# Kernel optimization log

Hardware: AMD Instinct MI355X
Metric: run time of the kernel (lower is better)

Reference implementation:

```python
import jax, jax.numpy as jnp
import numpy as np

B, S, TAGSET = 64, 512, 62
T = TAGSET + 2  # + START (index T-2) and END (index T-1)


def setup_inputs() -> dict:
    key = jax.random.key(0)
    k1, k2, k3, k4 = jax.random.split(key, 4)
    feats = jax.random.normal(k1, (B, S, T), dtype=jnp.float32)
    # transitions param (torch init is zeros; small random for a non-degenerate baseline)
    transitions = 0.01 * jax.random.normal(k2, (T, T), dtype=jnp.float32)
    # variable-length contiguous-prefix mask (CRF assumes mask[:, 0] == 1)
    lengths = jax.random.randint(k3, (B,), S // 2, S + 1)
    mask = (jnp.arange(S)[None, :] < lengths[:, None]).astype(jnp.int32)
    tags = jax.random.randint(k4, (B, S), 0, TAGSET).astype(jnp.int32)
    return {"feats": feats, "transitions": transitions, "mask": mask, "tags": tags}


def _nll(feats, transitions, mask, tags):
    b, s, t = feats.shape
    maskb = mask.astype(bool)
    feats_t = jnp.transpose(feats, (1, 0, 2))  # [S, B, T]
    mask_t = jnp.transpose(maskb, (1, 0))       # [S, B]

    # ---- partition function (calculate_PZ) ----
    start = t - 2
    init_part = feats_t[0] + transitions[start][None, :]  # [B, T]

    def step(part, inp):
        f_t, m_t = inp  # f_t: [B, T] emissions, m_t: [B]
        # scores[b, i, j] = part[b, i] + transitions[i, j] + f_t[b, j]
        cur = jax.nn.logsumexp(
            part[:, :, None] + transitions[None, :, :] + f_t[:, None, :], axis=1
        )  # [B, T]
        part = jnp.where(m_t[:, None], cur, part)
        return part, None

    part, _ = jax.lax.scan(step, init_part, (feats_t[1:], mask_t[1:]))
    final = jax.nn.logsumexp(part[:, :, None] + transitions[None, :, :], axis=1)
    forward_score = final[:, t - 1].sum()  # transition into END

    # ---- gold score (score_sentence) ----
    tags = tags.astype(jnp.int32)
    prev = jnp.concatenate(
        [jnp.full((b, 1), start, dtype=jnp.int32), tags[:, :-1]], axis=1
    )  # [B, S] previous tag (START at t=0)
    emit = jnp.take_along_axis(feats, tags[..., None].astype(jnp.int32), axis=2)[..., 0]
    trans = transitions[prev, tags]  # [B, S]
    tg_energy = jnp.where(maskb, emit + trans, 0.0).sum()
    lengths = mask.astype(jnp.int32).sum(axis=1)  # [B]
    end_ids = jnp.take_along_axis(tags, (lengths - 1)[:, None], axis=1)[:, 0]
    end_energy = transitions[end_ids, t - 1].sum()
    gold_score = tg_energy + end_energy

    return forward_score - gold_score


def reference(feats, transitions, mask, tags):
    return _nll(feats, transitions, mask, tags)
```

## Files before the change

### kernel.cpp

```cpp
#include <hip/hip_runtime.h>


#define SS 512
#define TT 64
#define CC 8
#define KCH 64
#define START_TAG 62
#define END_TAG 63
#define LOG2E_F 1.44269504088896340736f
#define LN2_F 0.69314718055994530942f

#define WS_ECOL_OFF 4194304
#define MSTR 72

typedef float v4f __attribute__((ext_vector_type(4)));
typedef _Float16 h4 __attribute__((ext_vector_type(4)));
typedef __fp16 c2 __attribute__((ext_vector_type(2)));
union H4u { h4 v; struct { c2 lo, hi; } p; };

__device__ __forceinline__ void cstep(const h4 (&A)[4][4], h4 (&B)[4],
                                      float* __restrict__ emb, float& fq,
                                      const float* __restrict__ fcol, int tload,
                                      int q, int l, int& esum, int& esc) {
    v4f z = {0.f, 0.f, 0.f, 0.f};
    v4f D[4];
#pragma unroll
    for (int mt = 0; mt < 4; ++mt) {
        v4f a = __builtin_amdgcn_mfma_f32_16x16x16f16(A[mt][0], B[0], z, 0, 0, 0);
        a = __builtin_amdgcn_mfma_f32_16x16x16f16(A[mt][1], B[1], a, 0, 0, 0);
        v4f b = __builtin_amdgcn_mfma_f32_16x16x16f16(A[mt][2], B[2], z, 0, 0, 0);
        b = __builtin_amdgcn_mfma_f32_16x16x16f16(A[mt][3], B[3], b, 0, 0, 0);
        D[mt] = a + b;
    }
    v4f em[4];
#pragma unroll
    for (int mt = 0; mt < 4; ++mt) em[mt] = *(const v4f*)(emb + 16 * mt + 4 * q);
    emb[l] = __builtin_amdgcn_exp2f(fq * LOG2E_F);
    fq = fcol[(size_t)tload * TT];
    esum += esc;
    float scf = __uint_as_float((unsigned)(127 - esc) << 23);
    v4f qs[4];
#pragma unroll
    for (int mt = 0; mt < 4; ++mt) qs[mt] = D[mt] * (em[mt] * scf);
#pragma unroll
    for (int mt = 0; mt < 4; ++mt) {
        H4u u;
        u.p.lo = __builtin_amdgcn_cvt_pkrtz(qs[mt].x, qs[mt].y);
        u.p.hi = __builtin_amdgcn_cvt_pkrtz(qs[mt].z, qs[mt].w);
        B[mt] = u.v;
    }
    unsigned u0 = (unsigned)__builtin_amdgcn_readfirstlane((int)__float_as_uint(qs[0].x));
    esc = (int)((u0 >> 23) & 255u) - 127;
}

__global__ __launch_bounds__(256, 1)
void crf_chunks(const float* __restrict__ feats, const float* __restrict__ trans,
                const int* __restrict__ mask, unsigned short* __restrict__ Pg,
                int* __restrict__ Eg, float* __restrict__ out) {
    __shared__ float em[4][4][2][TT];
    __shared__ __align__(16) _Float16 mldB[TT * MSTR];
    __shared__ __align__(16) _Float16 mldD[TT * MSTR];
    __shared__ int ebuf[12];

    const int blk = blockIdx.x;
    const int chain = blk >> 3, c = blk & 7;
    const int tid = threadIdx.x;
    const int w = tid >> 6, l = tid & 63;
    const int n16 = l & 15, q = l >> 4;
    const int ncol = 16 * w + n16;

    if (blk == 0 && tid == 0) out[0] = 0.f;

    h4 A[4][4];
#pragma unroll
    for (int mt = 0; mt < 4; ++mt)
#pragma unroll
        for (int ks = 0; ks < 4; ++ks) {
            h4 a;
#pragma unroll
            for (int e = 0; e < 4; ++e)
                a[e] = (_Float16)__builtin_amdgcn_exp2f(
                    trans[(16 * ks + 4 * q + e) * TT + 16 * mt + n16] * LOG2E_F);
            A[mt][ks] = a;
        }

    const int* mp = mask + chain * SS;
    int msum = 0;
#pragma unroll
    for (int k = 0; k < 8; ++k) msum += mp[k * 64 + l];
#pragma unroll
    for (int s_ = 1; s_ < 64; s_ <<= 1) msum += __shfl_xor(msum, s_, 64);
    const int L = msum;

    const int t0a = 1 + KCH * c;
    const int t0b = t0a + 16, t0c = t0a + 32, t0d = t0a + 48;
    const int base = (L - 1) - KCH * c;
    int nA = base < 0 ? 0 : (base > 16 ? 16 : base);
    int nB = base - 16 < 0 ? 0 : (base - 16 > 16 ? 16 : base - 16);
    int nC = base - 32 < 0 ? 0 : (base - 32 > 16 ? 16 : base - 32);
    int nD = base - 48 < 0 ? 0 : (base - 48 > 16 ? 16 : base - 48);

    h4 Ba[4], Bb[4], Bc[4], Bd[4];
#pragma unroll
    for (int ks = 0; ks < 4; ++ks) {
        h4 b;
#pragma unroll
        for (int jj = 0; jj < 4; ++jj)
            b[jj] = (_Float16)((16 * ks + 4 * q + jj == ncol) ? 1.f : 0.f);
        Ba[ks] = b; Bb[ks] = b; Bc[ks] = b; Bd[ks] = b;
    }

    const float* fcol = feats + (size_t)chain * SS * TT + l;
#define CT(x) ((x) < SS ? (x) : SS - 1)
    em[0][w][0][l] = __builtin_amdgcn_exp2f(fcol[(size_t)CT(t0a) * TT] * LOG2E_F);
    em[0][w][1][l] = __builtin_amdgcn_exp2f(fcol[(size_t)CT(t0a + 1) * TT] * LOG2E_F);
    em[1][w][0][l] = __builtin_amdgcn_exp2f(fcol[(size_t)CT(t0b) * TT] * LOG2E_F);
    em[1][w][1][l] = __builtin_amdgcn_exp2f(fcol[(size_t)CT(t0b + 1) * TT] * LOG2E_F);
    em[2][w][0][l] = __builtin_amdgcn_exp2f(fcol[(size_t)CT(t0c) * TT] * LOG2E_F);
    em[2][w][1][l] = __builtin_amdgcn_exp2f(fcol[(size_t)CT(t0c + 1) * TT] * LOG2E_F);
    em[3][w][0][l] = __builtin_amdgcn_exp2f(fcol[(size_t)CT(t0d) * TT] * LOG2E_F);
    em[3][w][1][l] = __builtin_amdgcn_exp2f(fcol[(size_t)CT(t0d + 1) * TT] * LOG2E_F);
    float fqA0 = fcol[(size_t)CT(t0a + 2) * TT];
    float fqA1 = fcol[(size_t)CT(t0a + 3) * TT];
    float fqB0 = fcol[(size_t)CT(t0b + 2) * TT];
    float fqB1 = fcol[(size_t)CT(t0b + 3) * TT];
    float fqC0 = fcol[(size_t)CT(t0c + 2) * TT];
    float fqC1 = fcol[(size_t)CT(t0c + 3) * TT];
    float fqD0 = fcol[(size_t)CT(t0d + 2) * TT];
    float fqD1 = fcol[(size_t)CT(t0d + 3) * TT];

    int esA = 0, escA = 0, esB = 0, escB = 0;
    int esC = 0, escC = 0, esD = 0, escD = 0;

    if (nD == 16) {
        for (int r = 0; r < 8; ++r) {
            const int s0 = 2 * r;
            cstep(A, Ba, &em[0][w][0][0], fqA0, fcol, CT(t0a + s0 + 4), q, l, esA, escA);
            cstep(A, Bb, &em[1][w][0][0], fqB0, fcol, CT(t0b + s0 + 4), q, l, esB, escB);
            cstep(A, Bc, &em[2][w][0][0], fqC0, fcol, CT(t0c + s0 + 4), q, l, esC, escC);
            cstep(A, Bd, &em[3][w][0][0], fqD0, fcol, CT(t0d + s0 + 4), q, l, esD, escD);
            cstep(A, Ba, &em[0][w][1][0], fqA1, fcol, CT(t0a + s0 + 5), q, l, esA, escA);
            cstep(A, Bb, &em[1][w][1][0], fqB1, fcol, CT(t0b + s0 + 5), q, l, esB, escB);
            cstep(A, Bc, &em[2][w][1][0], fqC1, fcol, CT(t0c + s0 + 5), q, l, esC, escC);
            cstep(A, Bd, &em[3][w][1][0], fqD1, fcol, CT(t0d + s0 + 5), q, l, esD, escD);
        }
    } else {
        for (int r = 0; r < 8; ++r) {
            const int s0 = 2 * r, s1 = s0 + 1;
            if (s0 < nA) cstep(A, Ba, &em[0][w][0][0], fqA0, fcol, CT(t0a + s0 + 4), q, l, esA, escA);
            if (s0 < nB) cstep(A, Bb, &em[1][w][0][0], fqB0, fcol, CT(t0b + s0 + 4), q, l, esB, escB);
            if (s0 < nC) cstep(A, Bc, &em[2][w][0][0], fqC0, fcol, CT(t0c + s0 + 4), q, l, esC, escC);
            if (s0 < nD) cstep(A, Bd, &em[3][w][0][0], fqD0, fcol, CT(t0d + s0 + 4), q, l, esD, escD);
            if (s1 < nA) cstep(A, Ba, &em[0][w][1][0], fqA1, fcol, CT(t0a + s1 + 4), q, l, esA, escA);
            if (s1 < nB) cstep(A, Bb, &em[1][w][1][0], fqB1, fcol, CT(t0b + s1 + 4), q, l, esB, escB);
            if (s1 < nC) cstep(A, Bc, &em[2][w][1][0], fqC1, fcol, CT(t0c + s1 + 4), q, l, esC, escC);
            if (s1 < nD) cstep(A, Bd, &em[3][w][1][0], fqD1, fcol, CT(t0d + s1 + 4), q, l, esD, escD);
        }
    }
#undef CT

    if (l == 0) { ebuf[w] = esB; ebuf[4 + w] = esD; }
    __syncthreads();
    const int eBmax = max(max(ebuf[0], ebuf[1]), max(ebuf[2], ebuf[3]));
    const int eDmax = max(max(ebuf[4], ebuf[5]), max(ebuf[6], ebuf[7]));
    {
        _Float16 sB = (_Float16)ldexpf(1.f, esB - eBmax);
        _Float16 sD = (_Float16)ldexpf(1.f, esD - eDmax);
        h4 s4B = {sB, sB, sB, sB}, s4D = {sD, sD, sD, sD};
#pragma unroll
        for (int ks = 0; ks < 4; ++ks) {
            h4 vb = Bb[ks] * s4B;
            h4 vd = Bd[ks] * s4D;
#pragma unroll
            for (int jj = 0; jj < 4; ++jj) {
                mldB[(16 * ks + 4 * q + jj) * MSTR + ncol] = vb[jj];
                mldD[(16 * ks + 4 * q + jj) * MSTR + ncol] = vd[jj];
            }
        }
    }
    __syncthreads();
    h4 AHb[4][4], AHd[4][4];
#pragma unroll
    for (int mt = 0; mt < 4; ++mt)
#pragma unroll
        for (int ks = 0; ks < 4; ++ks) {
            AHb[mt][ks] = *(const h4*)(mldB + (16 * mt + n16) * MSTR + 16 * ks + 4 * q);
            AHd[mt][ks] = *(const h4*)(mldD + (16 * mt + n16) * MSTR + 16 * ks + 4 * q);
        }
    v4f z = {0.f, 0.f, 0.f, 0.f};
    v4f P1[4], P2[4];
#pragma unroll
    for (int mt = 0; mt < 4; ++mt) {
        v4f a = __builtin_amdgcn_mfma_f32_16x16x16f16(AHb[mt][0], Ba[0], z, 0, 0, 0);
        a = __builtin_amdgcn_mfma_f32_16x16x16f16(AHb[mt][1], Ba[1], a, 0, 0, 0);
        v4f b = __builtin_amdgcn_mfma_f32_16x16x16f16(AHb[mt][2], Ba[2], z, 0, 0, 0);
        b = __builtin_amdgcn_mfma_f32_16x16x16f16(AHb[mt][3], Ba[3], b, 0, 0, 0);
        P1[mt] = a + b;
        v4f a2 = __builtin_amdgcn_mfma_f32_16x16x16f16(AHd[mt][0], Bc[0], z, 0, 0, 0);
        a2 = __builtin_amdgcn_mfma_f32_16x16x16f16(AHd[mt][1], Bc[1], a2, 0, 0, 0);
        v4f b2 = __builtin_amdgcn_mfma_f32_16x16x16f16(AHd[mt][2], Bc[2], z, 0, 0, 0);
        b2 = __builtin_amdgcn_mfma_f32_16x16x16f16(AHd[mt][3], Bc[3], b2, 0, 0, 0);
        P2[mt] = a2 + b2;
    }
    float m1 = 0.f, m2 = 0.f;
#pragma unroll
    for (int mt = 0; mt < 4; ++mt) {
        m1 = fmaxf(m1, fmaxf(fmaxf(P1[mt].x, P1[mt].y), fmaxf(P1[mt].z, P1[mt].w)));
        m2 = fmaxf(m2, fmaxf(fmaxf(P2[mt].x, P2[mt].y), fmaxf(P2[mt].z, P2[mt].w)));
    }
#pragma unroll
    for (int m = 1; m < 64; m <<= 1) {
        m1 = fmaxf(m1, __shfl_xor(m1, m, 64));
        m2 = fmaxf(m2, __shfl_xor(m2, m, 64));
    }
    unsigned u1 = (unsigned)__builtin_amdgcn_readfirstlane((int)__float_as_uint(m1));
    unsigned u2 = (unsigned)__builtin_amdgcn_readfirstlane((int)__float_as_uint(m2));
    const int e1c = u1 ? (int)((u1 >> 23) & 255u) - 127 : 0;
    const int e2c = u2 ? (int)((u2 >> 23) & 255u) - 127 : 0;
    const int e1 = esA + eBmax + e1c;
    const int e2 = esC + eDmax + e2c;
    h4 P1h[4], P2h[4];
    {
        float s1f = __uint_as_float((unsigned)(127 - e1c) << 23);
        float s2f = __uint_as_float((unsigned)(127 - e2c) << 23);
#pragma unroll
        for (int mt = 0; mt < 4; ++mt) {
            v4f q1 = P1[mt] * s1f;
            v4f q2 = P2[mt] * s2f;
            H4u ua, ub;
            ua.p.lo = __builtin_amdgcn_cvt_pkrtz(q1.x, q1.y);
            ua.p.hi = __builtin_amdgcn_cvt_pkrtz(q1.z, q1.w);
            ub.p.lo = __builtin_amdgcn_cvt_pkrtz(q2.x, q2.y);
            ub.p.hi = __builtin_amdgcn_cvt_pkrtz(q2.z, q2.w);
            P1h[mt] = ua.v;
            P2h[mt] = ub.v;
        }
    }

    if (l == 0) ebuf[8 + w] = e2;
    __syncthreads();
    const int e2max = max(max(ebuf[8], ebuf[9]), max(ebuf[10], ebuf[11]));
    {
        _Float16 s2 = (_Float16)ldexpf(1.f, e2 - e2max);
        h4 s4 = {s2, s2, s2, s2};
#pragma unroll
        for (int mt = 0; mt < 4; ++mt) {
            h4 v = P2h[mt] * s4;
#pragma unroll
            for (int jj = 0; jj < 4; ++jj)
                mldB[(16 * mt + 4 * q + jj) * MSTR + ncol] = v[jj];
        }
    }
    __syncthreads();
    h4 AHp[4][4];
#pragma unroll
    for (int mt = 0; mt < 4; ++mt)
#pragma unroll
        for (int ks = 0; ks < 4; ++ks)
            AHp[mt][ks] = *(const h4*)(mldB + (16 * mt + n16) * MSTR + 16 * ks + 4 * q);
    h4 Rf[4];
#pragma unroll
    for (int mt = 0; mt < 4; ++mt) {
        v4f a = __builtin_amdgcn_mfma_f32_16x16x16f16(AHp[mt][0], P1h[0], z, 0, 0, 0);
        a = __builtin_amdgcn_mfma_f32_16x16x16f16(AHp[mt][1], P1h[1], a, 0, 0, 0);
        v4f b = __builtin_amdgcn_mfma_f32_16x16x16f16(AHp[mt][2], P1h[2], z, 0, 0, 0);
        b = __builtin_amdgcn_mfma_f32_16x16x16f16(AHp[mt][3], P1h[3], b, 0, 0, 0);
        v4f d = a + b;
        H4u u;
        u.p.lo = __builtin_amdgcn_cvt_pkrtz(d.x, d.y);
        u.p.hi = __builtin_amdgcn_cvt_pkrtz(d.z, d.w);
        Rf[mt] = u.v;
    }
#pragma unroll
    for (int mt = 0; mt < 4; ++mt)
#pragma unroll
        for (int jj = 0; jj < 4; ++jj)
            mldD[(16 * mt + 4 * q + jj) * MSTR + ncol] = Rf[mt][jj];
    __syncthreads();
    {
        const size_t base_ = ((size_t)chain * CC + c) * 4096;
        int r = tid >> 2, cb = tid & 3;
        const uint4* src = (const uint4*)(mldD + r * MSTR + cb * 16);
        uint4* dst = (uint4*)(Pg + base_ + r * TT + cb * 16);
        dst[0] = src[0];
        dst[1] = src[1];
    }
    if (q == 0) Eg[(chain * CC + c) * TT + ncol] = e1 + eBmax == eBmax ? e1 + e2max : e1 + e2max;
}

__device__ __forceinline__ int wimax64(int v) {
#pragma unroll
    for (int m = 1; m < 64; m <<= 1) v = max(v, __shfl_xor(v, m, 64));
    return v;
}
__device__ __forceinline__ float wfmax64(float v) {
#pragma unroll
    for (int m = 1; m < 64; m <<= 1) v = fmaxf(v, __shfl_xor(v, m, 64));
    return v;
}
__device__ __forceinline__ float wfsum64(float v) {
#pragma unroll
    for (int m = 1; m < 64; m <<= 1) v += __shfl_xor(v, m, 64);
    return v;
}
__device__ __forceinline__ int fexp(float m) {
    unsigned u = (unsigned)__builtin_amdgcn_readfirstlane((int)__float_as_uint(m));
    return u ? (int)((u >> 23) & 255u) - 127 : 0;
}
__device__ __forceinline__ void mm64(const h4 (&A)[4][4], const h4 (&B)[4], v4f (&D)[4]) {
    v4f z = {0.f, 0.f, 0.f, 0.f};
#pragma unroll
    for (int mt = 0; mt < 4; ++mt) {
        v4f a = __builtin_amdgcn_mfma_f32_16x16x16f16(A[mt][0], B[0], z, 0, 0, 0);
        a = __builtin_amdgcn_mfma_f32_16x16x16f16(A[mt][1], B[1], a, 0, 0, 0);
        v4f b = __builtin_amdgcn_mfma_f32_16x16x16f16(A[mt][2], B[2], z, 0, 0, 0);
        b = __builtin_amdgcn_mfma_f32_16x16x16f16(A[mt][3], B[3], b, 0, 0, 0);
        D[mt] = a + b;
    }
}
__device__ __forceinline__ float dmax16(const v4f (&D)[4]) {
    float m = 0.f;
#pragma unroll
    for (int mt = 0; mt < 4; ++mt)
        m = fmaxf(m, fmaxf(fmaxf(D[mt].x, D[mt].y), fmaxf(D[mt].z, D[mt].w)));
    return m;
}
__device__ __forceinline__ void prodG(const unsigned short* __restrict__ PgC, int cA, int cB,
                                      const float* __restrict__ sAt,
                                      int n16, int q, int ncol, v4f (&D)[4]) {
    const _Float16* Ap = (const _Float16*)PgC + cA * 4096;
    const _Float16* Bp = (const _Float16*)PgC + cB * 4096;
    h4 Af[4][4];
#pragma unroll
    for (int mt = 0; mt < 4; ++mt)
#pragma unroll
        for (int ks = 0; ks < 4; ++ks) {
            h4 raw = *(const h4*)(Ap + (16 * mt + n16) * TT + 16 * ks + 4 * q);
            v4f s = *(const v4f*)(sAt + 16 * ks + 4 * q);
            h4 a;
#pragma unroll
            for (int e = 0; e < 4; ++e) a[e] = (_Float16)((float)raw[e] * s[e]);
            Af[mt][ks] = a;
        }
    h4 Bf[4];
#pragma unroll
    for (int ks = 0; ks < 4; ++ks) {
        h4 b;
#pragma unroll
        for (int j = 0; j < 4; ++j) b[j] = Bp[(16 * ks + 4 * q + j) * TT + ncol];
        Bf[ks] = b;
    }
    mm64(Af, Bf, D);
}

__global__ __launch_bounds__(256, 1)
void crf_combine(const float* __restrict__ feats, const float* __restrict__ trans,
                 const int* __restrict__ mask, const int* __restrict__ tags,
                 const unsigned short* __restrict__ Pg, const int* __restrict__ Eg,
                 float* __restrict__ out) {
    __shared__ __align__(16) _Float16 stg[TT * MSTR];
    __shared__ __align__(16) float sA[4][TT];
    __shared__ __align__(16) float wend[TT];
    __shared__ int eodd[4];
    __shared__ int ib0[4], ib1[4], ib2[4], ib3[4];
    __shared__ float redf[4], gred[4];

    const int chain = blockIdx.x;
    const int tid = threadIdx.x;
    const int w = tid >> 6, l = tid & 63;
    const int n16 = l & 15, q = l >> 4;
    const int ncol = 16 * w + n16;
    const unsigned short* PgC = Pg + (size_t)chain * CC * 4096;
    const int* EgC = Eg + chain * CC * TT;

    int msum = 0;
#pragma unroll
    for (int k = 0; k < 8; ++k) msum += mask[chain * SS + 64 * k + l];
    msum = wimax64(msum * 0 + msum);
    msum = 0;
#pragma unroll
    for (int k = 0; k < 8; ++k) msum += mask[chain * SS + 64 * k + l];
#pragma unroll
    for (int m = 1; m < 64; m <<= 1) msum += __shfl_xor(msum, m, 64);
    const int L = msum;

    float g = 0.f;
#pragma unroll
    for (int rep = 0; rep < 2; ++rep) {
        int t = tid + rep * 256;
        if (t < L) {
            int cur = tags[chain * SS + t];
            int prev = t ? tags[chain * SS + t - 1] : START_TAG;
            g += feats[(size_t)chain * SS * TT + (size_t)t * TT + cur] + trans[prev * TT + cur];
        }
    }
    g = wfsum64(g);
    if (l == 0) gred[w] = g;

    {
        int e1 = EgC[(2 * w + 1) * TT + l];
        int em = wimax64(e1);
        if (l == 0) eodd[w] = em;
        sA[w][l] = ldexpf(1.f, e1 - em);
    }
    if (tid < TT) wend[tid] = expf(trans[tid * TT + END_TAG]);
    __syncthreads();

    const float* f0 = feats + (size_t)chain * SS * TT;
    float pl = f0[l] + trans[START_TAG * TT + l];
    float M0 = wfmax64(pl);
    float pc = f0[ncol] + trans[START_TAG * TT + ncol];
    float p0c = __builtin_amdgcn_exp2f((pc - M0) * LOG2E_F);

    const int eqB0 = EgC[0 * TT + ncol];
    const int eqB1 = EgC[2 * TT + ncol];
    const int eqB2 = EgC[4 * TT + ncol];
    const int eqB3 = EgC[6 * TT + ncol];
    const int eo0 = eodd[0], eo1 = eodd[1], eo2 = eodd[2], eo3 = eodd[3];

    v4f D[4];
    prodG(PgC, 3, 2, &sA[1][0], n16, q, ncol, D);
    int ec1 = fexp(wfmax64(dmax16(D)));
    int eq1 = eqB1 + eo1 + ec1;
    if (l == 0) ib0[w] = 0;
    int eq1m = wimax64(eq1);
    if (l == 0) ib0[w] = eq1m;
    __syncthreads();
    const int emax1 = max(max(ib0[0], ib0[1]), max(ib0[2], ib0[3]));
    {
        float sc = ldexpf(1.f, eqB1 + eo1 - emax1);
#pragma unroll
        for (int mt = 0; mt < 4; ++mt)
#pragma unroll
            for (int jj = 0; jj < 4; ++jj)
                stg[(16 * mt + 4 * q + jj) * MSTR + ncol] = (_Float16)(D[mt][jj] * sc);
    }
    v4f D0[4];
    prodG(PgC, 1, 0, &sA[0][0], n16, q, ncol, D0);
    int ec0 = fexp(wfmax64(dmax16(D0)));
    int eq0 = eqB0 + eo0 + ec0;
    h4 Q0h[4];
    {
        float s0 = ldexpf(1.f, -ec0);
#pragma unroll
        for (int mt = 0; mt < 4; ++mt) {
            v4f qv = D0[mt] * s0;
            H4u u;
            u.p.lo = __builtin_amdgcn_cvt_pkrtz(qv.x, qv.y);
            u.p.hi = __builtin_amdgcn_cvt_pkrtz(qv.z, qv.w);
            Q0h[mt] = u.v;
        }
    }
    __syncthreads();
    h4 AH[4][4];
#pragma unroll
    for (int mt = 0; mt < 4; ++mt)
#pragma unroll
        for (int ks = 0; ks < 4; ++ks)
            AH[mt][ks] = *(const h4*)(stg + (16 * mt + n16) * MSTR + 16 * ks + 4 * q);
    v4f Dlo[4];
    mm64(AH, Q0h, Dlo);
    int eclo = fexp(wfmax64(dmax16(Dlo)));
    int eqlo = eq0 + emax1 + eclo;
    h4 Ploh[4];
    {
        float sl = ldexpf(1.f, -eclo);
#pragma unroll
        for (int mt = 0; mt < 4; ++mt) {
            v4f qv = Dlo[mt] * sl;
            H4u u;
            u.p.lo = __builtin_amdgcn_cvt_pkrtz(qv.x, qv.y);
            u.p.hi = __builtin_amdgcn_cvt_pkrtz(qv.z, qv.w);
            Ploh[mt] = u.v;
        }
    }
    prodG(PgC, 7, 6, &sA[3][0], n16, q, ncol, D);
    int ec3 = fexp(wfmax64(dmax16(D)));
    int eq3 = eqB3 + eo3 + ec3;
    int eq3m = wimax64(eq3);
    if (l == 0) ib1[w] = eq3m;
    __syncthreads();
    const int emax3 = max(max(ib1[0], ib1[1]), max(ib1[2], ib1[3]));
    {
        float sc = ldexpf(1.f, eqB3 + eo3 - emax3);
#pragma unroll
        for (int mt = 0; mt < 4; ++mt)
#pragma unroll
            for (int jj = 0; jj < 4; ++jj)
                stg[(16 * mt + 4 * q + jj) * MSTR + ncol] = (_Float16)(D[mt][jj] * sc);
    }
    v4f D2[4];
    prodG(PgC, 5, 4, &sA[2][0], n16, q, ncol, D2);
    int ec2 = fexp(wfmax64(dmax16(D2)));
    int eq2 = eqB2 + eo2 + ec2;
    h4 Q2h[4];
    {
        float s2 = ldexpf(1.f, -ec2);
#pragma unroll
        for (int mt = 0; mt < 4; ++mt) {
            v4f qv = D2[mt] * s2;
            H4u u;
            u.p.lo = __builtin_amdgcn_cvt_pkrtz(qv.x, qv.y);
            u.p.hi = __builtin_amdgcn_cvt_pkrtz(qv.z, qv.w);
            Q2h[mt] = u.v;
        }
    }
    __syncthreads();
#pragma unroll
    for (int mt = 0; mt < 4; ++mt)
#pragma unroll
        for (int ks = 0; ks < 4; ++ks)
            AH[mt][ks] = *(const h4*)(stg + (16 * mt + n16) * MSTR + 16 * ks + 4 * q);
    v4f Dhi[4];
    mm64(AH, Q2h, Dhi);
    int echi = fexp(wfmax64(dmax16(Dhi)));
    int eqhi = eq2 + emax3 + echi;
    int eqhim = wimax64(eqhi);
    if (l == 0) ib2[w] = eqhim;
    __syncthreads();
    const int emaxhi = max(max(ib2[0], ib2[1]), max(ib2[2], ib2[3]));
    {
        float sc = ldexpf(1.f, eq2 + emax3 - emaxhi);
#pragma unroll
        for (int mt = 0; mt < 4; ++mt)
#pragma unroll
            for (int jj = 0; jj < 4; ++jj)
                stg[(16 * mt + 4 * q + jj) * MSTR + ncol] = (_Float16)(Dhi[mt][jj] * sc);
    }
    __syncthreads();
#pragma unroll
    for (int mt = 0; mt < 4; ++mt)
#pragma unroll
        for (int ks = 0; ks < 4; ++ks)
            AH[mt][ks] = *(const h4*)(stg + (16 * mt + n16) * MSTR + 16 * ks + 4 * q);
    v4f DR[4];
    mm64(AH, Ploh, DR);

    float zsum = 0.f;
#pragma unroll
    for (int mt = 0; mt < 4; ++mt) {
        v4f wv = *(const v4f*)(wend + 16 * mt + 4 * q);
        zsum += wv.x * DR[mt].x + wv.y * DR[mt].y + wv.z * DR[mt].z + wv.w * DR[mt].w;
    }
    zsum += __shfl_xor(zsum, 16, 64);
    zsum += __shfl_xor(zsum, 32, 64);
    float val = zsum * p0c;
    int ex = eqlo + emaxhi;
    int exm = wimax64(ex);
    float contrib = (q == 0) ? ldexpf(val, ex - exm) : 0.f;
    float Sw = wfsum64(contrib);
    if (l == 0) { redf[w] = Sw; ib3[w] = exm; }
    __syncthreads();
    if (tid == 0) {
        int gmax = max(max(ib3[0], ib3[1]), max(ib3[2], ib3[3]));
        float tot = 0.f;
#pragma unroll
        for (int p = 0; p < 4; ++p) tot += ldexpf(redf[p], ib3[p] - gmax);
        float fwd = logf(tot) + (float)gmax * LN2_F + M0;
        float gold = gred[0] + gred[1] + gred[2] + gred[3] +
                     trans[tags[chain * SS + L - 1] * TT + END_TAG];
        atomicAdd(out, fwd - gold);
    }
}

extern "C" void kernel_launch(void* const* d_in, const int* in_sizes, int n_in,
                              void* d_out, int out_size, void* d_ws, size_t ws_size,
                              hipStream_t stream) {
    const float* feats = (const float*)d_in[0];
    const float* trans = (const float*)d_in[1];
    const int*   mask  = (const int*)d_in[2];
    const int*   tags  = (const int*)d_in[3];
    float* out = (float*)d_out;
    unsigned short* Pg = (unsigned short*)d_ws;
    int*       Eg = (int*)((char*)d_ws + WS_ECOL_OFF);

    crf_chunks<<<dim3(64 * CC), dim3(256), 0, stream>>>(feats, trans, mask, Pg, Eg, out);
    crf_combine<<<dim3(64), dim3(256), 0, stream>>>(feats, trans, mask, tags, Pg, Eg, out);
}
```

Before: 119.5 us.

## Fuse chunk and combine kernels via last-block atomic counter; preload emissions to LDS

Merges the per-chunk kernel and the combine kernel into one launch: each block bumps a per-chain atomic counter after writing its partial product, and the last block for the chain runs the combine step. Separately, all 64 emission rows per chunk are loaded up front with vectorized loads, exponentiated into shared memory, and then read by the step loop, replacing the rolling per-step prefetch. The aim is to remove one kernel launch and the gap between the two kernels, and to take global loads off the sequential critical path. In exchange it adds two memset calls, fences and a tail phase that runs on only one block per chain.

```diff
diff --git a/kernel.cpp b/kernel.cpp
--- a/kernel.cpp
+++ b/kernel.cpp
@@ -11,6 +11,7 @@
 #define LN2_F 0.69314718055994530942f
 
 #define WS_ECOL_OFF 4194304
+#define WS_CNT_OFF  4325376
 #define MSTR 72
 
 typedef float v4f __attribute__((ext_vector_type(4)));
@@ -18,10 +19,9 @@
 typedef __fp16 c2 __attribute__((ext_vector_type(2)));
 union H4u { h4 v; struct { c2 lo, hi; } p; };
 
-__device__ __forceinline__ void cstep(const h4 (&A)[4][4], h4 (&B)[4],
-                                      float* __restrict__ emb, float& fq,
-                                      const float* __restrict__ fcol, int tload,
-                                      int q, int l, int& esum, int& esc) {
+__device__ __forceinline__ void estep(const h4 (&A)[4][4], h4 (&B)[4],
+                                      const float* __restrict__ emrow,
+                                      int q, int& esum, int& esc) {
     v4f z = {0.f, 0.f, 0.f, 0.f};
     v4f D[4];
 #pragma unroll
@@ -32,16 +32,14 @@
         b = __builtin_amdgcn_mfma_f32_16x16x16f16(A[mt][3], B[3], b, 0, 0, 0);
         D[mt] = a + b;
     }
-    v4f em[4];
-#pragma unroll
-    for (int mt = 0; mt < 4; ++mt) em[mt] = *(const v4f*)(emb + 16 * mt + 4 * q);
-    emb[l] = __builtin_amdgcn_exp2f(fq * LOG2E_F);
-    fq = fcol[(size_t)tload * TT];
     esum += esc;
     float scf = __uint_as_float((unsigned)(127 - esc) << 23);
     v4f qs[4];
 #pragma unroll
-    for (int mt = 0; mt < 4; ++mt) qs[mt] = D[mt] * (em[mt] * scf);
+    for (int mt = 0; mt < 4; ++mt) {
+        v4f em = *(const v4f*)(emrow + 16 * mt + 4 * q);
+        qs[mt] = D[mt] * (em * scf);
+    }
 #pragma unroll
     for (int mt = 0; mt < 4; ++mt) {
         H4u u;
@@ -53,14 +51,86 @@
     esc = (int)((u0 >> 23) & 255u) - 127;
 }
 
+__device__ __forceinline__ int wimax64(int v) {
+#pragma unroll
+    for (int m = 1; m < 64; m <<= 1) v = max(v, __shfl_xor(v, m, 64));
+    return v;
+}
+__device__ __forceinline__ float wfmax64(float v) {
+#pragma unroll
+    for (int m = 1; m < 64; m <<= 1) v = fmaxf(v, __shfl_xor(v, m, 64));
+    return v;
+}
+__device__ __forceinline__ float wfsum64(float v) {
+#pragma unroll
+    for (int m = 1; m < 64; m <<= 1) v += __shfl_xor(v, m, 64);
+    return v;
+}
+__device__ __forceinline__ int fexp(float m) {
+    unsigned u = (unsigned)__builtin_amdgcn_readfirstlane((int)__float_as_uint(m));
+    return u ? (int)((u >> 23) & 255u) - 127 : 0;
+}
+__device__ __forceinline__ void mm64(const h4 (&A)[4][4], const h4 (&B)[4], v4f (&D)[4]) {
+    v4f z = {0.f, 0.f, 0.f, 0.f};
+#pragma unroll
+    for (int mt = 0; mt < 4; ++mt) {
+        v4f a = __builtin_amdgcn_mfma_f32_16x16x16f16(A[mt][0], B[0], z, 0, 0, 0);
+        a = __builtin_amdgcn_mfma_f32_16x16x16f16(A[mt][1], B[1], a, 0, 0, 0);
+        v4f b = __builtin_amdgcn_mfma_f32_16x16x16f16(A[mt][2], B[2], z, 0, 0, 0);
+        b = __builtin_amdgcn_mfma_f32_16x16x16f16(A[mt][3], B[3], b, 0, 0, 0);
+        D[mt] = a + b;
+    }
+}
+__device__ __forceinline__ float dmax16(const v4f (&D)[4]) {
+    float m = 0.f;
+#pragma unroll
+    for (int mt = 0; mt < 4; ++mt)
+        m = fmaxf(m, fmaxf(fmaxf(D[mt].x, D[mt].y), fmaxf(D[mt].z, D[mt].w)));
+    return m;
+}
+__device__ __forceinline__ void prodG(const unsigned short* __restrict__ PgC, int cA, int cB,
+                                      const float* __restrict__ sAt,
+                                      int n16, int q, int ncol, v4f (&D)[4]) {
+    const _Float16* Ap = (const _Float16*)PgC + cA * 4096;
+    const _Float16* Bp = (const _Float16*)PgC + cB * 4096;
+    h4 Af[4][4];
+#pragma unroll
+    for (int mt = 0; mt < 4; ++mt)
+#pragma unroll
+        for (int ks = 0; ks < 4; ++ks) {
+            h4 raw = *(const h4*)(Ap + (16 * mt + n16) * TT + 16 * ks + 4 * q);
+            v4f s = *(const v4f*)(sAt + 16 * ks + 4 * q);
+            h4 a;
+#pragma unroll
+            for (int e = 0; e < 4; ++e) a[e] = (_Float16)((float)raw[e] * s[e]);
+            Af[mt][ks] = a;
+        }
+    h4 Bf[4];
+#pragma unroll
+    for (int ks = 0; ks < 4; ++ks) {
+        h4 b;
+#pragma unroll
+        for (int j = 0; j < 4; ++j) b[j] = Bp[(16 * ks + 4 * q + j) * TT + ncol];
+        Bf[ks] = b;
+    }
+    mm64(Af, Bf, D);
+}
+
 __global__ __launch_bounds__(256, 1)
-void crf_chunks(const float* __restrict__ feats, const float* __restrict__ trans,
-                const int* __restrict__ mask, unsigned short* __restrict__ Pg,
-                int* __restrict__ Eg, float* __restrict__ out) {
-    __shared__ float em[4][4][2][TT];
+void crf_fused(const float* __restrict__ feats, const float* __restrict__ trans,
+               const int* __restrict__ mask, const int* __restrict__ tags,
+               unsigned short* __restrict__ Pg, int* __restrict__ Eg,
+               unsigned* __restrict__ cnt, float* __restrict__ out) {
+    __shared__ __align__(16) float emS[KCH][TT];
     __shared__ __align__(16) _Float16 mldB[TT * MSTR];
     __shared__ __align__(16) _Float16 mldD[TT * MSTR];
     __shared__ int ebuf[12];
+    __shared__ int lastf;
+    __shared__ __align__(16) float sA[4][TT];
+    __shared__ __align__(16) float wend[TT];
+    __shared__ int eodd[4];
+    __shared__ int ib0[4], ib1[4], ib2[4], ib3[4];
+    __shared__ float redf[4], gred[4];
 
     const int blk = blockIdx.x;
     const int chain = blk >> 3, c = blk & 7;
@@ -69,8 +139,6 @@
     const int n16 = l & 15, q = l >> 4;
     const int ncol = 16 * w + n16;
 
-    if (blk == 0 && tid == 0) out[0] = 0.f;
-
     h4 A[4][4];
 #pragma unroll
     for (int mt = 0; mt < 4; ++mt)
@@ -93,13 +161,29 @@
     const int L = msum;
 
     const int t0a = 1 + KCH * c;
-    const int t0b = t0a + 16, t0c = t0a + 32, t0d = t0a + 48;
     const int base = (L - 1) - KCH * c;
     int nA = base < 0 ? 0 : (base > 16 ? 16 : base);
     int nB = base - 16 < 0 ? 0 : (base - 16 > 16 ? 16 : base - 16);
     int nC = base - 32 < 0 ? 0 : (base - 32 > 16 ? 16 : base - 32);
     int nD = base - 48 < 0 ? 0 : (base - 48 > 16 ? 16 : base - 48);
 
+    const float* fbase = feats + (size_t)chain * SS * TT;
+#pragma unroll
+    for (int k = 0; k < 4; ++k) {
+        int idx = tid + 256 * k;
+        int row = idx >> 4;
+        int seg = idx & 15;
+        int t = t0a + row;
+        t = t < SS ? t : SS - 1;
+        v4f v = *(const v4f*)(fbase + (size_t)t * TT + 4 * seg);
+        v4f e;
+        e.x = __builtin_amdgcn_exp2f(v.x * LOG2E_F);
+        e.y = __builtin_amdgcn_exp2f(v.y * LOG2E_F);
+        e.z = __builtin_amdgcn_exp2f(v.z * LOG2E_F);
+        e.w = __builtin_amdgcn_exp2f(v.w * LOG2E_F);
+        *(v4f*)(&emS[row][4 * seg]) = e;
+    }
+
     h4 Ba[4], Bb[4], Bc[4], Bd[4];
 #pragma unroll
     for (int ks = 0; ks < 4; ++ks) {
@@ -109,25 +193,7 @@
             b[jj] = (_Float16)((16 * ks + 4 * q + jj == ncol) ? 1.f : 0.f);
         Ba[ks] = b; Bb[ks] = b; Bc[ks] = b; Bd[ks] = b;
     }
-
-    const float* fcol = feats + (size_t)chain * SS * TT + l;
-#define CT(x) ((x) < SS ? (x) : SS - 1)
-    em[0][w][0][l] = __builtin_amdgcn_exp2f(fcol[(size_t)CT(t0a) * TT] * LOG2E_F);
-    em[0][w][1][l] = __builtin_amdgcn_exp2f(fcol[(size_t)CT(t0a + 1) * TT] * LOG2E_F);
-    em[1][w][0][l] = __builtin_amdgcn_exp2f(fcol[(size_t)CT(t0b) * TT] * LOG2E_F);
-    em[1][w][1][l] = __builtin_amdgcn_exp2f(fcol[(size_t)CT(t0b + 1) * TT] * LOG2E_F);
-    em[2][w][0][l] = __builtin_amdgcn_exp2f(fcol[(size_t)CT(t0c) * TT] * LOG2E_F);
-    em[2][w][1][l] = __builtin_amdgcn_exp2f(fcol[(size_t)CT(t0c + 1) * TT] * LOG2E_F);
-    em[3][w][0][l] = __builtin_amdgcn_exp2f(fcol[(size_t)CT(t0d) * TT] * LOG2E_F);
-    em[3][w][1][l] = __builtin_amdgcn_exp2f(fcol[(size_t)CT(t0d + 1) * TT] * LOG2E_F);
-    float fqA0 = fcol[(size_t)CT(t0a + 2) * TT];
-    float fqA1 = fcol[(size_t)CT(t0a + 3) * TT];
-    float fqB0 = fcol[(size_t)CT(t0b + 2) * TT];
-    float fqB1 = fcol[(size_t)CT(t0b + 3) * TT];
-    float fqC0 = fcol[(size_t)CT(t0c + 2) * TT];
-    float fqC1 = fcol[(size_t)CT(t0c + 3) * TT];
-    float fqD0 = fcol[(size_t)CT(t0d + 2) * TT];
-    float fqD1 = fcol[(size_t)CT(t0d + 3) * TT];
+    __syncthreads();
 
     int esA = 0, escA = 0, esB = 0, escB = 0;
     int esC = 0, escC = 0, esD = 0, escD = 0;
@@ -135,29 +201,28 @@
     if (nD == 16) {
         for (int r = 0; r < 8; ++r) {
             const int s0 = 2 * r;
-            cstep(A, Ba, &em[0][w][0][0], fqA0, fcol, CT(t0a + s0 + 4), q, l, esA, escA);
-            cstep(A, Bb, &em[1][w][0][0], fqB0, fcol, CT(t0b + s0 + 4), q, l, esB, escB);
-            cstep(A, Bc, &em[2][w][0][0], fqC0, fcol, CT(t0c + s0 + 4), q, l, esC, escC);
-            cstep(A, Bd, &em[3][w][0][0], fqD0, fcol, CT(t0d + s0 + 4), q, l, esD, escD);
-            cstep(A, Ba, &em[0][w][1][0], fqA1, fcol, CT(t0a + s0 + 5), q, l, esA, escA);
-            cstep(A, Bb, &em[1][w][1][0], fqB1, fcol, CT(t0b + s0 + 5), q, l, esB, escB);
-            cstep(A, Bc, &em[2][w][1][0], fqC1, fcol, CT(t0c + s0 + 5), q, l, esC, escC);
-            cstep(A, Bd, &em[3][w][1][0], fqD1, fcol, CT(t0d + s0 + 5), q, l, esD, escD);
+            estep(A, Ba, &emS[s0][0],      q, esA, escA);
+            estep(A, Bb, &emS[16 + s0][0], q, esB, escB);
+            estep(A, Bc, &emS[32 + s0][0], q, esC, escC);
+            estep(A, Bd, &emS[48 + s0][0], q, esD, escD);
+            estep(A, Ba, &emS[s0 + 1][0],      q, esA, escA);
+            estep(A, Bb, &emS[17 + s0][0], q, esB, escB);
+            estep(A, Bc, &emS[33 + s0][0], q, esC, escC);
+            estep(A, Bd, &emS[49 + s0][0], q, esD, escD);
         }
     } else {
         for (int r = 0; r < 8; ++r) {
             const int s0 = 2 * r, s1 = s0 + 1;
-            if (s0 < nA) cstep(A, Ba, &em[0][w][0][0], fqA0, fcol, CT(t0a + s0 + 4), q, l, esA, escA);
-            if (s0 < nB) cstep(A, Bb, &em[1][w][0][0], fqB0, fcol, CT(t0b + s0 + 4), q, l, esB, escB);
-            if (s0 < nC) cstep(A, Bc, &em[2][w][0][0], fqC0, fcol, CT(t0c + s0 + 4), q, l, esC, escC);
-            if (s0 < nD) cstep(A, Bd, &em[3][w][0][0], fqD0, fcol, CT(t0d + s0 + 4), q, l, esD, escD);
-            if (s1 < nA) cstep(A, Ba, &em[0][w][1][0], fqA1, fcol, CT(t0a + s1 + 4), q, l, esA, escA);
-            if (s1 < nB) cstep(A, Bb, &em[1][w][1][0], fqB1, fcol, CT(t0b + s1 + 4), q, l, esB, escB);
-            if (s1 < nC) cstep(A, Bc, &em[2][w][1][0], fqC1, fcol, CT(t0c + s1 + 4), q, l, esC, escC);
-            if (s1 < nD) cstep(A, Bd, &em[3][w][1][0], fqD1, fcol, CT(t0d + s1 + 4), q, l, esD, escD);
-        }
-    }
-#undef CT
+            if (s0 < nA) estep(A, Ba, &emS[s0][0],      q, esA, escA);
+            if (s0 < nB) estep(A, Bb, &emS[16 + s0][0], q, esB, escB);
+            if (s0 < nC) estep(A, Bc, &emS[32 + s0][0], q, esC, escC);
+            if (s0 < nD) estep(A, Bd, &emS[48 + s0][0], q, esD, escD);
+            if (s1 < nA) estep(A, Ba, &emS[s1][0],      q, esA, escA);
+            if (s1 < nB) estep(A, Bb, &emS[16 + s1][0], q, esB, escB);
+            if (s1 < nC) estep(A, Bc, &emS[32 + s1][0], q, esC, escC);
+            if (s1 < nD) estep(A, Bd, &emS[48 + s1][0], q, esD, escD);
+        }
+    }
 
     if (l == 0) { ebuf[w] = esB; ebuf[4 + w] = esD; }
     __syncthreads();
@@ -271,6 +336,7 @@
         u.p.hi = __builtin_amdgcn_cvt_pkrtz(d.z, d.w);
         Rf[mt] = u.v;
     }
+    __syncthreads();
 #pragma unroll
     for (int mt = 0; mt < 4; ++mt)
 #pragma unroll
@@ -285,104 +351,20 @@
         dst[0] = src[0];
         dst[1] = src[1];
     }
-    if (q == 0) Eg[(chain * CC + c) * TT + ncol] = e1 + eBmax == eBmax ? e1 + e2max : e1 + e2max;
-}
-
-__device__ __forceinline__ int wimax64(int v) {
-#pragma unroll
-    for (int m = 1; m < 64; m <<= 1) v = max(v, __shfl_xor(v, m, 64));
-    return v;
-}
-__device__ __forceinline__ float wfmax64(float v) {
-#pragma unroll
-    for (int m = 1; m < 64; m <<= 1) v = fmaxf(v, __shfl_xor(v, m, 64));
-    return v;
-}
-__device__ __forceinline__ float wfsum64(float v) {
-#pragma unroll
-    for (int m = 1; m < 64; m <<= 1) v += __shfl_xor(v, m, 64);
-    return v;
-}
-__device__ __forceinline__ int fexp(float m) {
-    unsigned u = (unsigned)__builtin_amdgcn_readfirstlane((int)__float_as_uint(m));
-    return u ? (int)((u >> 23) & 255u) - 127 : 0;
-}
-__device__ __forceinline__ void mm64(const h4 (&A)[4][4], const h4 (&B)[4], v4f (&D)[4]) {
-    v4f z = {0.f, 0.f, 0.f, 0.f};
-#pragma unroll
-    for (int mt = 0; mt < 4; ++mt) {
-        v4f a = __builtin_amdgcn_mfma_f32_16x16x16f16(A[mt][0], B[0], z, 0, 0, 0);
-        a = __builtin_amdgcn_mfma_f32_16x16x16f16(A[mt][1], B[1], a, 0, 0, 0);
-        v4f b = __builtin_amdgcn_mfma_f32_16x16x16f16(A[mt][2], B[2], z, 0, 0, 0);
-        b = __builtin_amdgcn_mfma_f32_16x16x16f16(A[mt][3], B[3], b, 0, 0, 0);
-        D[mt] = a + b;
-    }
-}
-__device__ __forceinline__ float dmax16(const v4f (&D)[4]) {
-    float m = 0.f;
-#pragma unroll
-    for (int mt = 0; mt < 4; ++mt)
-        m = fmaxf(m, fmaxf(fmaxf(D[mt].x, D[mt].y), fmaxf(D[mt].z, D[mt].w)));
-    return m;
-}
-__device__ __forceinline__ void prodG(const unsigned short* __restrict__ PgC, int cA, int cB,
-                                      const float* __restrict__ sAt,
-                                      int n16, int q, int ncol, v4f (&D)[4]) {
-    const _Float16* Ap = (const _Float16*)PgC + cA * 4096;
-    const _Float16* Bp = (const _Float16*)PgC + cB * 4096;
-    h4 Af[4][4];
-#pragma unroll
-    for (int mt = 0; mt < 4; ++mt)
-#pragma unroll
-        for (int ks = 0; ks < 4; ++ks) {
-            h4 raw = *(const h4*)(Ap + (16 * mt + n16) * TT + 16 * ks + 4 * q);
-            v4f s = *(const v4f*)(sAt + 16 * ks + 4 * q);
-            h4 a;
-#pragma unroll
-            for (int e = 0; e < 4; ++e) a[e] = (_Float16)((float)raw[e] * s[e]);
-            Af[mt][ks] = a;
-        }
-    h4 Bf[4];
-#pragma unroll
-    for (int ks = 0; ks < 4; ++ks) {
-        h4 b;
-#pragma unroll
-        for (int j = 0; j < 4; ++j) b[j] = Bp[(16 * ks + 4 * q + j) * TT + ncol];
-        Bf[ks] = b;
-    }
-    mm64(Af, Bf, D);
-}
-
-__global__ __launch_bounds__(256, 1)
-void crf_combine(const float* __restrict__ feats, const float* __restrict__ trans,
-                 const int* __restrict__ mask, const int* __restrict__ tags,
-                 const unsigned short* __restrict__ Pg, const int* __restrict__ Eg,
-                 float* __restrict__ out) {
-    __shared__ __align__(16) _Float16 stg[TT * MSTR];
-    __shared__ __align__(16) float sA[4][TT];
-    __shared__ __align__(16) float wend[TT];
-    __shared__ int eodd[4];
-    __shared__ int ib0[4], ib1[4], ib2[4], ib3[4];
-    __shared__ float redf[4], gred[4];
-
-    const int chain = blockIdx.x;
-    const int tid = threadIdx.x;
-    const int w = tid >> 6, l = tid & 63;
-    const int n16 = l & 15, q = l >> 4;
-    const int ncol = 16 * w + n16;
+    if (q == 0) Eg[(chain * CC + c) * TT + ncol] = e1 + e2max;
+
+    __syncthreads();
+    __threadfence();
+    if (tid == 0) {
+        unsigned old = atomicAdd(&cnt[chain], 1u);
+        lastf = (old == (unsigned)(CC - 1));
+    }
+    __syncthreads();
+    if (!lastf) return;
+    __threadfence();
+
     const unsigned short* PgC = Pg + (size_t)chain * CC * 4096;
     const int* EgC = Eg + chain * CC * TT;
-
-    int msum = 0;
-#pragma unroll
-    for (int k = 0; k < 8; ++k) msum += mask[chain * SS + 64 * k + l];
-    msum = wimax64(msum * 0 + msum);
-    msum = 0;
-#pragma unroll
-    for (int k = 0; k < 8; ++k) msum += mask[chain * SS + 64 * k + l];
-#pragma unroll
-    for (int m = 1; m < 64; m <<= 1) msum += __shfl_xor(msum, m, 64);
-    const int L = msum;
 
     float g = 0.f;
 #pragma unroll
@@ -391,25 +373,24 @@
         if (t < L) {
             int cur = tags[chain * SS + t];
             int prev = t ? tags[chain * SS + t - 1] : START_TAG;
-            g += feats[(size_t)chain * SS * TT + (size_t)t * TT + cur] + trans[prev * TT + cur];
+            g += fbase[(size_t)t * TT + cur] + trans[prev * TT + cur];
         }
     }
     g = wfsum64(g);
     if (l == 0) gred[w] = g;
 
     {
-        int e1 = EgC[(2 * w + 1) * TT + l];
-        int em = wimax64(e1);
+        int e1t = EgC[(2 * w + 1) * TT + l];
+        int em = wimax64(e1t);
         if (l == 0) eodd[w] = em;
-        sA[w][l] = ldexpf(1.f, e1 - em);
+        sA[w][l] = ldexpf(1.f, e1t - em);
     }
     if (tid < TT) wend[tid] = expf(trans[tid * TT + END_TAG]);
     __syncthreads();
 
-    const float* f0 = feats + (size_t)chain * SS * TT;
-    float pl = f0[l] + trans[START_TAG * TT + l];
+    float pl = fbase[l] + trans[START_TAG * TT + l];
     float M0 = wfmax64(pl);
-    float pc = f0[ncol] + trans[START_TAG * TT + ncol];
+    float pc = fbase[ncol] + trans[START_TAG * TT + ncol];
     float p0c = __builtin_amdgcn_exp2f((pc - M0) * LOG2E_F);
 
     const int eqB0 = EgC[0 * TT + ncol];
@@ -422,7 +403,6 @@
     prodG(PgC, 3, 2, &sA[1][0], n16, q, ncol, D);
     int ec1 = fexp(wfmax64(dmax16(D)));
     int eq1 = eqB1 + eo1 + ec1;
-    if (l == 0) ib0[w] = 0;
     int eq1m = wimax64(eq1);
     if (l == 0) ib0[w] = eq1m;
     __syncthreads();
@@ -433,7 +413,7 @@
         for (int mt = 0; mt < 4; ++mt)
 #pragma unroll
             for (int jj = 0; jj < 4; ++jj)
-                stg[(16 * mt + 4 * q + jj) * MSTR + ncol] = (_Float16)(D[mt][jj] * sc);
+                mldB[(16 * mt + 4 * q + jj) * MSTR + ncol] = (_Float16)(D[mt][jj] * sc);
     }
     v4f D0[4];
     prodG(PgC, 1, 0, &sA[0][0], n16, q, ncol, D0);
@@ -457,7 +437,7 @@
     for (int mt = 0; mt < 4; ++mt)
 #pragma unroll
         for (int ks = 0; ks < 4; ++ks)
-            AH[mt][ks] = *(const h4*)(stg + (16 * mt + n16) * MSTR + 16 * ks + 4 * q);
+            AH[mt][ks] = *(const h4*)(mldB + (16 * mt + n16) * MSTR + 16 * ks + 4 * q);
     v4f Dlo[4];
     mm64(AH, Q0h, Dlo);
     int eclo = fexp(wfmax64(dmax16(Dlo)));
@@ -487,7 +467,7 @@
         for (int mt = 0; mt < 4; ++mt)
 #pragma unroll
             for (int jj = 0; jj < 4; ++jj)
-                stg[(16 * mt + 4 * q + jj) * MSTR + ncol] = (_Float16)(D[mt][jj] * sc);
+                mldB[(16 * mt + 4 * q + jj) * MSTR + ncol] = (_Float16)(D[mt][jj] * sc);
     }
     v4f D2[4];
     prodG(PgC, 5, 4, &sA[2][0], n16, q, ncol, D2);
@@ -510,7 +490,7 @@
     for (int mt = 0; mt < 4; ++mt)
 #pragma unroll
         for (int ks = 0; ks < 4; ++ks)
-            AH[mt][ks] = *(const h4*)(stg + (16 * mt + n16) * MSTR + 16 * ks + 4 * q);
+            AH[mt][ks] = *(const h4*)(mldB + (16 * mt + n16) * MSTR + 16 * ks + 4 * q);
     v4f Dhi[4];
     mm64(AH, Q2h, Dhi);
     int echi = fexp(wfmax64(dmax16(Dhi)));
@@ -525,14 +505,14 @@
         for (int mt = 0; mt < 4; ++mt)
 #pragma unroll
             for (int jj = 0; jj < 4; ++jj)
-                stg[(16 * mt + 4 * q + jj) * MSTR + ncol] = (_Float16)(Dhi[mt][jj] * sc);
+                mldB[(16 * mt + 4 * q + jj) * MSTR + ncol] = (_Float16)(Dhi[mt][jj] * sc);
     }
     __syncthreads();
 #pragma unroll
     for (int mt = 0; mt < 4; ++mt)
 #pragma unroll
         for (int ks = 0; ks < 4; ++ks)
-            AH[mt][ks] = *(const h4*)(stg + (16 * mt + n16) * MSTR + 16 * ks + 4 * q);
+            AH[mt][ks] = *(const h4*)(mldB + (16 * mt + n16) * MSTR + 16 * ks + 4 * q);
     v4f DR[4];
     mm64(AH, Ploh, DR);
 
@@ -572,8 +552,10 @@
     const int*   tags  = (const int*)d_in[3];
     float* out = (float*)d_out;
     unsigned short* Pg = (unsigned short*)d_ws;
-    int*       Eg = (int*)((char*)d_ws + WS_ECOL_OFF);
-
-    crf_chunks<<<dim3(64 * CC), dim3(256), 0, stream>>>(feats, trans, mask, Pg, Eg, out);
-    crf_combine<<<dim3(64), dim3(256), 0, stream>>>(feats, trans, mask, tags, Pg, Eg, out);
-}
+    int*       Eg  = (int*)((char*)d_ws + WS_ECOL_OFF);
+    unsigned*  cnt = (unsigned*)((char*)d_ws + WS_CNT_OFF);
+
+    hipMemsetAsync((char*)d_ws + WS_CNT_OFF, 0, 64 * sizeof(unsigned), stream);
+    hipMemsetAsync(d_out, 0, sizeof(float), stream);
+    crf_fused<<<dim3(64 * CC), dim3(256), 0, stream>>>(feats, trans, mask, tags, Pg, Eg, cnt, out);
+}
```

After: 187.6 us. 57.0% more time.
